# Performance work log

Measured on AMD Instinct MI355X. Metric: run time of the kernel, lower is better.

Reference implementation:

```python
import jax, jax.numpy as jnp
import numpy as np

N_NODES = 50000
N_EDGES = 1600000
IN_DIM = 128
OUT_DIM = 16
N_HEADS = 8


def setup_inputs() -> dict:
    key = jax.random.key(0)
    ks = jax.random.split(key, 9)
    s = 1.0 / np.sqrt(IN_DIM)
    return {
        "h": jax.random.normal(ks[0], (N_NODES, IN_DIM), jnp.float32),
        "Wq": jax.random.normal(ks[1], (IN_DIM, OUT_DIM * N_HEADS), jnp.float32) * s,
        "bq": jax.random.normal(ks[2], (OUT_DIM * N_HEADS,), jnp.float32) * 0.01,
        "Wk": jax.random.normal(ks[3], (IN_DIM, OUT_DIM * N_HEADS), jnp.float32) * s,
        "bk": jax.random.normal(ks[4], (OUT_DIM * N_HEADS,), jnp.float32) * 0.01,
        "Wv": jax.random.normal(ks[5], (IN_DIM, OUT_DIM * N_HEADS), jnp.float32) * s,
        "bv": jax.random.normal(ks[6], (OUT_DIM * N_HEADS,), jnp.float32) * 0.01,
        "src": jax.random.randint(ks[7], (N_EDGES,), 0, N_NODES, jnp.int32),
        "dst": jax.random.randint(ks[8], (N_EDGES,), 0, N_NODES, jnp.int32),
    }


def reference(h, Wq, bq, Wk, bk, Wv, bv, src, dst):
    n_nodes = h.shape[0]
    # node-wise Q/K/V projections -> [N, H, D]
    Q = (h @ Wq + bq).reshape(n_nodes, N_HEADS, OUT_DIM)
    K = (h @ Wk + bk).reshape(n_nodes, N_HEADS, OUT_DIM)
    V = (h @ Wv + bv).reshape(n_nodes, N_HEADS, OUT_DIM)
    # edge-wise score: (K[src] * Q[dst]).sum(-1), scaled-exp with clamp
    score = jnp.sum(K[src] * Q[dst], axis=-1)  # [E, H]
    score = jnp.exp(jnp.clip(score / np.sqrt(OUT_DIM), -5.0, 5.0))
    # scatter-sum weighted values and normalizers to dst nodes
    msg = V[src] * score[:, :, None]  # [E, H, D]
    wV = jax.ops.segment_sum(msg, dst, num_segments=n_nodes)  # [N, H, D]
    z = jax.ops.segment_sum(score, dst, num_segments=n_nodes)  # [N, H]
    return wV / (z[:, :, None] + 1e-6)
```

## Files before the change

kernel.cpp:

```cpp
#include <hip/hip_runtime.h>
#include <hip/hip_bf16.h>
#include <cstddef>

#define N_NODES 50000
#define N_EDGES 1600000
#define IN_DIM 128
#define OUT_DIM 16
#define N_HEADS 8
#define QKV_DIM 128
#define HS_STRIDE 136
#define OS_STRIDE 392

#define SUBB 3125
#define BCAP 1024
#define BH_CHUNK 8192
#define BH_BLOCKS 196
#define GEMM_BLOCKS 782
#define FUSED_BLOCKS (BH_BLOCKS + GEMM_BLOCKS)

typedef __hip_bfloat16 bf16;
typedef short bf16x8 __attribute__((ext_vector_type(8)));
typedef float f32x4  __attribute__((ext_vector_type(4)));

__device__ __forceinline__ float b2f(bf16 x) { return __bfloat162float(x); }

__device__ __forceinline__ float u16tof(unsigned int u) {
    unsigned int x = u << 16;
    float f;
    __builtin_memcpy(&f, &x, 4);
    return f;
}

__device__ __forceinline__ unsigned short f2bf(float v) {
    bf16 b = __float2bfloat16(v);
    unsigned short u;
    __builtin_memcpy(&u, &b, 2);
    return u;
}

__global__ __launch_bounds__(256) void sentinel_kernel(unsigned short* __restrict__ out, int n) {
    int i = blockIdx.x * 256 + threadIdx.x;
    if (i < n) out[i] = 0x42C8;
}

__global__ __launch_bounds__(256) void prep_kernel(
    const unsigned short* __restrict__ hraw,
    const void* __restrict__ Wqr, const void* __restrict__ bqr,
    const void* __restrict__ Wkr, const void* __restrict__ bkr,
    const void* __restrict__ Wvr, const void* __restrict__ bvr,
    int* __restrict__ flag,
    unsigned short* __restrict__ Wfrag, float* __restrict__ bias_f)
{
    __shared__ int red[256];
    const int t   = threadIdx.x;
    const int tid = blockIdx.x * 256 + t;

    int cnt = 0;
    for (int i = t; i < 8192; i += 256) {
        unsigned short u = hraw[i];
        int e = (u >> 7) & 0xFF;
        if (e == 0xFF || e > 0x85 || (e == 0 && (u & 0x7F) != 0)) cnt++;
    }
    red[t] = cnt;
    __syncthreads();
    for (int s = 128; s > 0; s >>= 1) {
        if (t < s) red[t] += red[t + s];
        __syncthreads();
    }
    const bool f32 = (red[0] > 100);
    if (blockIdx.x == 0 && t == 0) *flag = red[0];

    if (tid < 384) {
        int mat = tid >> 7, c = tid & 127;
        const void* bp = (mat == 0) ? bqr : (mat == 1) ? bkr : bvr;
        bias_f[tid] = f32 ? ((const float*)bp)[c] : b2f(((const bf16*)bp)[c]);
    }

    int l  = tid & 63;
    int s  = (tid >> 6) & 3;
    int nt = tid >> 8;
    int n  = nt * 16 + (l & 15);
    int k0 = s * 32 + (l >> 4) * 8;
    int mat = n >> 7, c = n & 127;
    const void* Wp = (mat == 0) ? Wqr : (mat == 1) ? Wkr : Wvr;

    unsigned short v[8];
#pragma unroll
    for (int j = 0; j < 8; ++j) {
        int k = k0 + j;
        float w = f32 ? ((const float*)Wp)[k * QKV_DIM + c]
                      : b2f(((const bf16*)Wp)[k * QKV_DIM + c]);
        v[j] = f2bf(w);
    }
    ushort4* o = (ushort4*)(Wfrag + (size_t)tid * 8);
    o[0] = make_ushort4(v[0], v[1], v[2], v[3]);
    o[1] = make_ushort4(v[4], v[5], v[6], v[7]);
}

__global__ __launch_bounds__(256) void fused_gs_kernel(
    const void* __restrict__ hraw,
    const unsigned short* __restrict__ Wfrag, const float* __restrict__ bias_f,
    const int* __restrict__ flag,
    unsigned short* __restrict__ Qt, unsigned short* __restrict__ KVt,
    const int* __restrict__ src, const int* __restrict__ dst,
    unsigned int* __restrict__ packed, unsigned int* __restrict__ offcnt)
{
    __shared__ __align__(16) unsigned char arena[64 * OS_STRIDE * 2];
    const int t = threadIdx.x;

    if (blockIdx.x < BH_BLOCKS) {
        int* lcnt           = (int*)arena;
        unsigned int* stage = (unsigned int*)(arena + 12544);
        int* sm             = (int*)(arena + 45312);

        const int b    = blockIdx.x;
        const int base = b * BH_CHUNK;
        const int nb   = min(N_EDGES - base, BH_CHUNK);

        for (int i = t; i < SUBB; i += 256) lcnt[i] = 0;
        __syncthreads();

        for (int i = t; i < nb; i += 256)
            atomicAdd(&lcnt[dst[base + i] >> 4], 1);
        __syncthreads();

        {
            const int lane = t & 63;
            const int wave = t >> 6;
            const int i0   = t * 13;

            int xs[13];
            int ssum = 0;
#pragma unroll
            for (int j = 0; j < 13; ++j) {
                int i = i0 + j;
                int x = (i < SUBB) ? lcnt[i] : 0;
                xs[j] = x;
                ssum += x;
            }
            int v = ssum;
#pragma unroll
            for (int sh = 1; sh < 64; sh <<= 1) {
                int a = __shfl_up(v, sh);
                if (lane >= sh) v += a;
            }
            if (lane == 63) sm[wave] = v;
            __syncthreads();
            int run = v - ssum;
#pragma unroll
            for (int w = 0; w < 4; ++w)
                if (w < wave) run += sm[w];
#pragma unroll
            for (int j = 0; j < 13; ++j) {
                int i = i0 + j;
                if (i < SUBB) {
                    offcnt[(size_t)b * SUBB + i] =
                        ((unsigned int)run << 16) | (unsigned int)xs[j];
                    lcnt[i] = run;
                    run += xs[j];
                }
            }
            __syncthreads();
        }

        for (int i = t; i < nb; i += 256) {
            int d = dst[base + i];
            int bk = d >> 4;
            int pos = atomicAdd(&lcnt[bk], 1);
            stage[pos] = (unsigned int)src[base + i] | ((unsigned int)(d & 15) << 16);
        }
        __syncthreads();

        for (int i = t; i < nb; i += 256)
            packed[base + i] = stage[i];

    } else {
        unsigned short* smem = (unsigned short*)arena;

        const bool f32 = (*flag > 100);
        const int m0 = (blockIdx.x - BH_BLOCKS) * 64;

#pragma unroll
        for (int it = 0; it < 8; ++it) {
            int idx = it * 1024 + t * 4;
            int r = idx >> 7, k = idx & 127;
            int row = m0 + r;
            ushort4 w4 = make_ushort4(0, 0, 0, 0);
            if (row < N_NODES) {
                if (f32) {
                    float4 v4 = ((const float4*)hraw)[(size_t)row * 32 + (k >> 2)];
                    w4 = make_ushort4(f2bf(v4.x), f2bf(v4.y), f2bf(v4.z), f2bf(v4.w));
                } else {
                    uint2 u = ((const uint2*)hraw)[(size_t)row * 32 + (k >> 2)];
                    w4 = make_ushort4((unsigned short)(u.x & 0xffffu), (unsigned short)(u.x >> 16),
                                      (unsigned short)(u.y & 0xffffu), (unsigned short)(u.y >> 16));
                }
            }
            *(ushort4*)&smem[r * HS_STRIDE + k] = w4;
        }
        __syncthreads();

        const int lane = t & 63;
        const int wave = t >> 6;
        const int qd   = lane >> 4;
        const int ln15 = lane & 15;

        bf16x8 afr[4][4];
#pragma unroll
        for (int ms = 0; ms < 4; ++ms)
#pragma unroll
            for (int s = 0; s < 4; ++s)
                afr[ms][s] = *(const bf16x8*)&smem[(ms * 16 + ln15) * HS_STRIDE + s * 32 + qd * 8];

        __syncthreads();

#pragma unroll
        for (int i = 0; i < 6; ++i) {
            const int nt  = wave + i * 4;
            const int col = nt * 16 + ln15;
            const float bs = bias_f[col];
            const int mat = col >> 7, c127 = col & 127;
            const int ocol = (mat == 0) ? c127
                           : 128 + 8 * (c127 >> 2) + (c127 & 3) + ((mat == 2) ? 4 : 0);

            bf16x8 bfr[4];
#pragma unroll
            for (int s = 0; s < 4; ++s)
                bfr[s] = *(const bf16x8*)(Wfrag + ((size_t)(nt * 4 + s) * 64 + lane) * 8);

#pragma unroll
            for (int ms = 0; ms < 4; ++ms) {
                f32x4 acc = {0.f, 0.f, 0.f, 0.f};
#pragma unroll
                for (int s = 0; s < 4; ++s)
                    acc = __builtin_amdgcn_mfma_f32_16x16x32_bf16(afr[ms][s], bfr[s], acc, 0, 0, 0);
#pragma unroll
                for (int r = 0; r < 4; ++r) {
                    int rl = ms * 16 + qd * 4 + r;
                    smem[rl * OS_STRIDE + ocol] = f2bf(acc[r] + bs);
                }
            }
        }
        __syncthreads();

        for (int q = t; q < 1024; q += 256) {
            int row = q >> 4, c = q & 15;
            int grow = m0 + row;
            if (grow < N_NODES)
                ((uint4*)Qt)[grow * 16 + c] = *(const uint4*)&smem[row * OS_STRIDE + c * 8];
        }
        for (int q = t; q < 2048; q += 256) {
            int row = q >> 5, g = q & 31;
            int grow = m0 + row;
            if (grow < N_NODES)
                ((uint4*)KVt)[grow * 32 + g] = *(const uint4*)&smem[row * OS_STRIDE + 128 + g * 8];
        }
    }
}

__global__ __launch_bounds__(256) void bucket_agg_kernel(
    const unsigned short* __restrict__ Qt, const unsigned short* __restrict__ KVt,
    const unsigned int* __restrict__ packed, const unsigned int* __restrict__ offcnt,
    const int* __restrict__ flag, void* __restrict__ out)
{
    __shared__ unsigned int   lds_pk[BCAP];
    __shared__ unsigned short lds_src[BCAP];
    __shared__ int runoff[BH_BLOCKS], runcnt[BH_BLOCKS], runpfx[BH_BLOCKS];
    __shared__ int cnt16[16], base16[16], cur16[16];
    __shared__ int wsum[4];
    __shared__ int nb_s;

    const int sb = blockIdx.x;
    const int t  = threadIdx.x;

    if (t < 16) { cnt16[t] = 0; cur16[t] = 0; }
    if (t < BH_BLOCKS) {
        unsigned int oc = offcnt[(size_t)t * SUBB + sb];
        runoff[t] = t * BH_CHUNK + (int)(oc >> 16);
        runcnt[t] = (int)(oc & 0xffffu);
    }
    __syncthreads();

    {
        const int lane = t & 63;
        const int wv   = t >> 6;
        int x = (t < BH_BLOCKS) ? runcnt[t] : 0;
        int v = x;
#pragma unroll
        for (int sh = 1; sh < 64; sh <<= 1) {
            int a = __shfl_up(v, sh);
            if (lane >= sh) v += a;
        }
        if (lane == 63) wsum[wv] = v;
        __syncthreads();
#pragma unroll
        for (int w = 0; w < 4; ++w)
            if (w < wv) v += wsum[w];
        if (t < BH_BLOCKS) runpfx[t] = v - x;
        if (t == 0) nb_s = wsum[0] + wsum[1] + wsum[2] + wsum[3];
        __syncthreads();
    }
    const int nb = min(nb_s, BCAP);

    for (int r = t; r < BH_BLOCKS; r += 256) {
        int ro = runoff[r], rc = runcnt[r], rp = runpfx[r];
        for (int j = 0; j < rc; ++j) {
            int dpos = rp + j;
            if (dpos < BCAP) {
                unsigned int pk = packed[ro + j];
                lds_pk[dpos] = pk;
                atomicAdd(&cnt16[(pk >> 16) & 15], 1);
            }
        }
    }
    __syncthreads();
    if (t == 0) {
        int acc = 0;
#pragma unroll
        for (int i = 0; i < 16; ++i) { base16[i] = acc; acc += cnt16[i]; }
    }
    __syncthreads();
    for (int j = t; j < nb; j += 256) {
        unsigned int pk = lds_pk[j];
        int dl = (pk >> 16) & 15;
        int pos = base16[dl] + atomicAdd(&cur16[dl], 1);
        lds_src[pos] = (unsigned short)(pk & 0xffffu);
    }
    __syncthreads();

    const int wave = t >> 6;
    const int lane = t & 63;
    const int half = lane >> 5;
    const int hl   = lane & 31;
    const uint4* KV4 = (const uint4*)KVt;
    const bool of32 = (*flag > 100);

    for (int dl = wave; dl < 16; dl += 4) {
        const int d = sb * 16 + dl;
        uint2 qw = ((const uint2*)Qt)[d * 32 + hl];
        const float q0 = u16tof(qw.x & 0xffffu), q1 = u16tof(qw.x >> 16);
        const float q2 = u16tof(qw.y & 0xffffu), q3 = u16tof(qw.y >> 16);
        const int off = base16[dl];
        const int n   = cnt16[dl];

        float a0 = 0.f, a1 = 0.f, a2 = 0.f, a3 = 0.f, zz = 0.f;

#define CONSUME(KV, SCMASK)                                                     \
        {                                                                       \
            float p = fmaf(u16tof((KV).x & 0xffffu), q0,                        \
                      fmaf(u16tof((KV).x >> 16), q1,                            \
                      fmaf(u16tof((KV).y & 0xffffu), q2,                        \
                           u16tof((KV).y >> 16) * q3)));                        \
            p += __shfl_xor(p, 1);                                              \
            p += __shfl_xor(p, 2);                                              \
            float sc = __expf(__builtin_amdgcn_fmed3f(p * 0.25f, -5.f, 5.f));   \
            sc *= (SCMASK);                                                     \
            a0 = fmaf(u16tof((KV).z & 0xffffu), sc, a0);                        \
            a1 = fmaf(u16tof((KV).z >> 16),     sc, a1);                        \
            a2 = fmaf(u16tof((KV).w & 0xffffu), sc, a2);                        \
            a3 = fmaf(u16tof((KV).w >> 16),     sc, a3);                        \
            zz += sc;                                                           \
        }

        int j = 0;
        for (; j + 16 <= n; j += 16) {
            int e[8];
#pragma unroll
            for (int u = 0; u < 8; ++u) e[u] = lds_src[off + j + 2 * u + half];
            uint4 kv[8];
#pragma unroll
            for (int u = 0; u < 8; ++u) kv[u] = KV4[e[u] * 32 + hl];
#pragma unroll
            for (int u = 0; u < 8; ++u) CONSUME(kv[u], 1.f)
        }
        if (j + 8 <= n) {
            int e[4];
#pragma unroll
            for (int u = 0; u < 4; ++u) e[u] = lds_src[off + j + 2 * u + half];
            uint4 kv[4];
#pragma unroll
            for (int u = 0; u < 4; ++u) kv[u] = KV4[e[u] * 32 + hl];
#pragma unroll
            for (int u = 0; u < 4; ++u) CONSUME(kv[u], 1.f)
            j += 8;
        }
        for (; j + 2 <= n; j += 2) {
            int e = lds_src[off + j + half];
            uint4 kv = KV4[e * 32 + hl];
            CONSUME(kv, 1.f)
        }
        if (j < n) {
            int e = lds_src[off + j];
            uint4 kv = KV4[e * 32 + hl];
            CONSUME(kv, (half == 0) ? 1.f : 0.f)
        }
#undef CONSUME

        a0 += __shfl_xor(a0, 32);
        a1 += __shfl_xor(a1, 32);
        a2 += __shfl_xor(a2, 32);
        a3 += __shfl_xor(a3, 32);
        zz += __shfl_xor(zz, 32);

        const float inv = 1.f / (zz + 1e-6f);
        const float r0 = a0 * inv, r1 = a1 * inv, r2 = a2 * inv, r3 = a3 * inv;

        if (half == 0) {
            if (of32) {
                ((float4*)out)[d * 32 + hl] = make_float4(r0, r1, r2, r3);
            } else {
                unsigned int w0 = ((unsigned int)f2bf(r1) << 16) | f2bf(r0);
                unsigned int w1 = ((unsigned int)f2bf(r3) << 16) | f2bf(r2);
                ((uint2*)out)[d * 32 + hl] = make_uint2(w0, w1);
            }
        }
    }
}

extern "C" void kernel_launch(void* const* d_in, const int* in_sizes, int n_in,
                              void* d_out, int out_size, void* d_ws, size_t ws_size,
                              hipStream_t stream)
{
    const void* h  = d_in[0];
    const void* Wq = d_in[1];
    const void* bq = d_in[2];
    const void* Wk = d_in[3];
    const void* bk = d_in[4];
    const void* Wv = d_in[5];
    const void* bv = d_in[6];
    const int*  src = (const int*)d_in[7];
    const int*  dst = (const int*)d_in[8];

    const size_t NQ = (size_t)N_NODES * QKV_DIM;
    const size_t WFRAG_N = 24 * 4 * 64 * 8;
    const size_t PACKED_N = (size_t)BH_BLOCKS * BH_CHUNK;
    const size_t OFFCNT_N = (size_t)BH_BLOCKS * SUBB;

    const size_t need = 3 * NQ * 2 + WFRAG_N * 2 + 384 * 4 + 64
                      + PACKED_N * 4 + OFFCNT_N * 4;

    if (ws_size < need) {
        sentinel_kernel<<<(out_size + 255) / 256, 256, 0, stream>>>((unsigned short*)d_out, out_size);
        return;
    }

    unsigned short* Qt  = (unsigned short*)d_ws;
    unsigned short* KVt = Qt + NQ;
    unsigned short* Wfrag = KVt + 2 * NQ;
    float* bias_f = (float*)(Wfrag + WFRAG_N);
    int* flag     = (int*)(bias_f + 384);
    unsigned int* packed = (unsigned int*)(flag + 16);
    unsigned int* offcnt = packed + PACKED_N;

    prep_kernel<<<24, 256, 0, stream>>>((const unsigned short*)h,
        Wq, bq, Wk, bk, Wv, bv, flag, Wfrag, bias_f);

    fused_gs_kernel<<<FUSED_BLOCKS, 256, 0, stream>>>(h, Wfrag, bias_f, flag,
        Qt, KVt, src, dst, packed, offcnt);

    bucket_agg_kernel<<<SUBB, 256, 0, stream>>>(Qt, KVt, packed, offcnt, flag, d_out);
}
```

Baseline: 251.5 us.

## Shrink fused kernel LDS footprint and raise aggregation occupancy

The fused histogram/GEMM kernel's shared arena shrinks from a 64x392 output tile to a 64x136 input tile. The GEMM now writes Q, K and V in three passes through the same buffer, storing KV interleaved as uint2 halves. The bucket stage drops its LDS staging array and scatters packed entries directly to global memory. The aggregation kernel gets launch_bounds(256,8) and a smaller unroll (8 edges instead of 16) to cut register pressure and raise occupancy. In exchange it adds extra barriers in the GEMM, makes global writes for the packed array uncoalesced, and exposes less memory-level parallelism per wave.

```diff
diff --git a/kernel.cpp b/kernel.cpp
--- a/kernel.cpp
+++ b/kernel.cpp
@@ -9,12 +9,12 @@
 #define N_HEADS 8
 #define QKV_DIM 128
 #define HS_STRIDE 136
-#define OS_STRIDE 392
 
 #define SUBB 3125
 #define BCAP 1024
 #define BH_CHUNK 8192
 #define BH_BLOCKS 196
+#define GEMM_M 64
 #define GEMM_BLOCKS 782
 #define FUSED_BLOCKS (BH_BLOCKS + GEMM_BLOCKS)
 
@@ -105,13 +105,12 @@
     const int* __restrict__ src, const int* __restrict__ dst,
     unsigned int* __restrict__ packed, unsigned int* __restrict__ offcnt)
 {
-    __shared__ __align__(16) unsigned char arena[64 * OS_STRIDE * 2];
+    __shared__ __align__(16) unsigned char arena[GEMM_M * HS_STRIDE * 2];
     const int t = threadIdx.x;
 
     if (blockIdx.x < BH_BLOCKS) {
-        int* lcnt           = (int*)arena;
-        unsigned int* stage = (unsigned int*)(arena + 12544);
-        int* sm             = (int*)(arena + 45312);
+        int* lcnt = (int*)arena;
+        int* sm   = (int*)(arena + 12544);
 
         const int b    = blockIdx.x;
         const int base = b * BH_CHUNK;
@@ -167,18 +166,14 @@
             int d = dst[base + i];
             int bk = d >> 4;
             int pos = atomicAdd(&lcnt[bk], 1);
-            stage[pos] = (unsigned int)src[base + i] | ((unsigned int)(d & 15) << 16);
-        }
-        __syncthreads();
-
-        for (int i = t; i < nb; i += 256)
-            packed[base + i] = stage[i];
+            packed[base + pos] = (unsigned int)src[base + i] | ((unsigned int)(d & 15) << 16);
+        }
 
     } else {
         unsigned short* smem = (unsigned short*)arena;
 
         const bool f32 = (*flag > 100);
-        const int m0 = (blockIdx.x - BH_BLOCKS) * 64;
+        const int m0 = (blockIdx.x - BH_BLOCKS) * GEMM_M;
 
 #pragma unroll
         for (int it = 0; it < 8; ++it) {
@@ -215,50 +210,56 @@
         __syncthreads();
 
 #pragma unroll
-        for (int i = 0; i < 6; ++i) {
-            const int nt  = wave + i * 4;
-            const int col = nt * 16 + ln15;
-            const float bs = bias_f[col];
-            const int mat = col >> 7, c127 = col & 127;
-            const int ocol = (mat == 0) ? c127
-                           : 128 + 8 * (c127 >> 2) + (c127 & 3) + ((mat == 2) ? 4 : 0);
-
-            bf16x8 bfr[4];
-#pragma unroll
-            for (int s = 0; s < 4; ++s)
-                bfr[s] = *(const bf16x8*)(Wfrag + ((size_t)(nt * 4 + s) * 64 + lane) * 8);
-
-#pragma unroll
-            for (int ms = 0; ms < 4; ++ms) {
-                f32x4 acc = {0.f, 0.f, 0.f, 0.f};
+        for (int p = 0; p < 3; ++p) {
+#pragma unroll
+            for (int ii = 0; ii < 2; ++ii) {
+                const int i   = 2 * p + ii;
+                const int nt  = wave + i * 4;
+                const int col = nt * 16 + ln15;
+                const float bs = bias_f[col];
+                const int c127 = col & 127;
+
+                bf16x8 bfr[4];
 #pragma unroll
                 for (int s = 0; s < 4; ++s)
-                    acc = __builtin_amdgcn_mfma_f32_16x16x32_bf16(afr[ms][s], bfr[s], acc, 0, 0, 0);
-#pragma unroll
-                for (int r = 0; r < 4; ++r) {
-                    int rl = ms * 16 + qd * 4 + r;
-                    smem[rl * OS_STRIDE + ocol] = f2bf(acc[r] + bs);
+                    bfr[s] = *(const bf16x8*)(Wfrag + ((size_t)(nt * 4 + s) * 64 + lane) * 8);
+
+#pragma unroll
+                for (int ms = 0; ms < 4; ++ms) {
+                    f32x4 acc = {0.f, 0.f, 0.f, 0.f};
+#pragma unroll
+                    for (int s = 0; s < 4; ++s)
+                        acc = __builtin_amdgcn_mfma_f32_16x16x32_bf16(afr[ms][s], bfr[s], acc, 0, 0, 0);
+#pragma unroll
+                    for (int r = 0; r < 4; ++r) {
+                        int rl = ms * 16 + qd * 4 + r;
+                        smem[rl * HS_STRIDE + c127] = f2bf(acc[r] + bs);
+                    }
                 }
             }
-        }
-        __syncthreads();
-
-        for (int q = t; q < 1024; q += 256) {
-            int row = q >> 4, c = q & 15;
-            int grow = m0 + row;
-            if (grow < N_NODES)
-                ((uint4*)Qt)[grow * 16 + c] = *(const uint4*)&smem[row * OS_STRIDE + c * 8];
-        }
-        for (int q = t; q < 2048; q += 256) {
-            int row = q >> 5, g = q & 31;
-            int grow = m0 + row;
-            if (grow < N_NODES)
-                ((uint4*)KVt)[grow * 32 + g] = *(const uint4*)&smem[row * OS_STRIDE + 128 + g * 8];
-        }
-    }
-}
-
-__global__ __launch_bounds__(256) void bucket_agg_kernel(
+            __syncthreads();
+            if (p == 0) {
+                for (int q = t; q < 1024; q += 256) {
+                    int row = q >> 4, c = q & 15;
+                    int grow = m0 + row;
+                    if (grow < N_NODES)
+                        ((uint4*)Qt)[grow * 16 + c] = *(const uint4*)&smem[row * HS_STRIDE + c * 8];
+                }
+            } else {
+                for (int q = t; q < 2048; q += 256) {
+                    int row = q >> 5, g = q & 31;
+                    int grow = m0 + row;
+                    if (grow < N_NODES)
+                        ((uint2*)KVt)[(size_t)grow * 64 + g * 2 + (p - 1)] =
+                            *(const uint2*)&smem[row * HS_STRIDE + g * 4];
+                }
+            }
+            __syncthreads();
+        }
+    }
+}
+
+__global__ __launch_bounds__(256, 8) void bucket_agg_kernel(
     const unsigned short* __restrict__ Qt, const unsigned short* __restrict__ KVt,
     const unsigned int* __restrict__ packed, const unsigned int* __restrict__ offcnt,
     const int* __restrict__ flag, void* __restrict__ out)
@@ -341,7 +342,7 @@
         const float q0 = u16tof(qw.x & 0xffffu), q1 = u16tof(qw.x >> 16);
         const float q2 = u16tof(qw.y & 0xffffu), q3 = u16tof(qw.y >> 16);
         const int off = base16[dl];
-        const int n   = cnt16[dl];
+        const int nd  = cnt16[dl];
 
         float a0 = 0.f, a1 = 0.f, a2 = 0.f, a3 = 0.f, zz = 0.f;
 
@@ -363,17 +364,7 @@
         }
 
         int j = 0;
-        for (; j + 16 <= n; j += 16) {
-            int e[8];
-#pragma unroll
-            for (int u = 0; u < 8; ++u) e[u] = lds_src[off + j + 2 * u + half];
-            uint4 kv[8];
-#pragma unroll
-            for (int u = 0; u < 8; ++u) kv[u] = KV4[e[u] * 32 + hl];
-#pragma unroll
-            for (int u = 0; u < 8; ++u) CONSUME(kv[u], 1.f)
-        }
-        if (j + 8 <= n) {
+        for (; j + 8 <= nd; j += 8) {
             int e[4];
 #pragma unroll
             for (int u = 0; u < 4; ++u) e[u] = lds_src[off + j + 2 * u + half];
@@ -382,14 +373,13 @@
             for (int u = 0; u < 4; ++u) kv[u] = KV4[e[u] * 32 + hl];
 #pragma unroll
             for (int u = 0; u < 4; ++u) CONSUME(kv[u], 1.f)
-            j += 8;
-        }
-        for (; j + 2 <= n; j += 2) {
+        }
+        for (; j + 2 <= nd; j += 2) {
             int e = lds_src[off + j + half];
             uint4 kv = KV4[e * 32 + hl];
             CONSUME(kv, 1.f)
         }
-        if (j < n) {
+        if (j < nd) {
             int e = lds_src[off + j];
             uint4 kv = KV4[e * 32 + hl];
             CONSUME(kv, (half == 0) ? 1.f : 0.f)
```

New measurement: 253.9 us. No clear change (+0.9%).
